# Optimization experiments

Measured on AMD Instinct MI355X. Metric: run time of the kernel, lower is better.

The kernel has to match this reference:

```python
import jax, jax.numpy as jnp
import numpy as np

N_EMBD = 128
N_HEADS = 8
HEAD_SIZE = N_EMBD // N_HEADS  # 16
EPS = 1e-5


def _layernorm(x, g, b):
    m = jnp.mean(x, axis=-1, keepdims=True)
    v = jnp.mean(jnp.square(x - m), axis=-1, keepdims=True)
    return (x - m) * jax.lax.rsqrt(v + EPS) * g + b


def setup_inputs() -> dict:
    key = jax.random.key(0)
    ks = jax.random.split(key, 12)
    B, T, D, H, HS = 16, 1024, N_EMBD, N_HEADS, HEAD_SIZE
    s = 1.0 / np.sqrt(D)
    inp = {
        "x": jax.random.normal(ks[0], (B, T, D), jnp.float32),
        # per-head QKV projections (stacked over heads; matches ModuleList of Linear(D, HS))
        "Wq": jax.random.uniform(ks[1], (H, D, HS), jnp.float32, -s, s),
        "bq": jnp.zeros((H, HS), jnp.float32),
        "Wk": jax.random.uniform(ks[2], (H, D, HS), jnp.float32, -s, s),
        "bk": jnp.zeros((H, HS), jnp.float32),
        "Wv": jax.random.uniform(ks[3], (H, D, HS), jnp.float32, -s, s),
        "bv": jnp.zeros((H, HS), jnp.float32),
        "Wp": jax.random.uniform(ks[4], (H * HS, D), jnp.float32, -s, s),
        "bp": jnp.zeros((D,), jnp.float32),
        "W1": jax.random.uniform(ks[5], (D, 4 * D), jnp.float32, -s, s),
        "b1": jnp.zeros((4 * D,), jnp.float32),
        "W2": jax.random.uniform(ks[6], (4 * D, D), jnp.float32, -1.0 / np.sqrt(4 * D), 1.0 / np.sqrt(4 * D)),
        "b2": jnp.zeros((D,), jnp.float32),
        "g1": jnp.ones((D,), jnp.float32),
        "be1": jnp.zeros((D,), jnp.float32),
        "g2": jnp.ones((D,), jnp.float32),
        "be2": jnp.zeros((D,), jnp.float32),
    }
    return inp


def reference(x, Wq, bq, Wk, bk, Wv, bv, Wp, bp, W1, b1, W2, b2, g1, be1, g2, be2):
    B, T, D = x.shape
    # batched per-head projections: [B,T,D] x [H,D,HS] -> [B,H,T,HS]
    q = jnp.einsum("btd,hds->bhts", x, Wq) + bq[None, :, None, :]
    k = jnp.einsum("btd,hds->bhts", x, Wk) + bk[None, :, None, :]
    v = jnp.einsum("btd,hds->bhts", x, Wv) + bv[None, :, None, :]
    scores = jnp.einsum("bhts,bhus->bhtu", q, k) / np.sqrt(HEAD_SIZE).astype(np.float32)
    tril = jnp.tril(jnp.ones((T, T), x.dtype))
    # faithful to source: multiplicative + additive mask (not -inf where)
    scores = scores * tril - 1e12 * (1.0 - tril)
    attn = jax.nn.softmax(scores, axis=-1)
    out = jnp.einsum("bhtu,bhus->bhts", attn, v)  # [B,H,T,HS]
    # concat heads in head order -> [B,T,H*HS]
    out = out.transpose(0, 2, 1, 3).reshape(B, T, -1)
    attn_out = out @ Wp + bp
    x = _layernorm(attn_out + x, g1, be1)
    h = jax.nn.gelu(x @ W1 + b1, approximate=False) @ W2 + b2
    x = _layernorm(h + x, g2, be2)
    return x
```

## Files before the change

kernel.cpp:

```cpp
#include <hip/hip_runtime.h>
#include <hip/hip_bf16.h>
#include <math.h>

constexpr int NB  = 16;
constexpr int NT  = 1024;
constexpr int ND  = 128;
constexpr int NH  = 8;
constexpr int NHS = 16;
constexpr int NDH = 512;
constexpr long NBT = (long)NB * NT;

typedef __attribute__((ext_vector_type(8))) short short8;
typedef __attribute__((ext_vector_type(4))) float f32x4;
typedef __attribute__((ext_vector_type(4))) unsigned short us4;

__device__ __forceinline__ unsigned short f2bf(float f) {
    __hip_bfloat16 h = __float2bfloat16(f);
    return *(unsigned short*)&h;
}
__device__ __forceinline__ float b2f(unsigned short u) {
    union { unsigned int i; float f; } t;
    t.i = ((unsigned int)u) << 16;
    return t.f;
}

__device__ __forceinline__ short8 cvt8(const float* p) {
    const float4 f0 = *(const float4*)p;
    const float4 f1 = *(const float4*)(p + 4);
    union { short8 s; __hip_bfloat162 h[4]; } u;
    u.h[0] = __float22bfloat162_rn(make_float2(f0.x, f0.y));
    u.h[1] = __float22bfloat162_rn(make_float2(f0.z, f0.w));
    u.h[2] = __float22bfloat162_rn(make_float2(f1.x, f1.y));
    u.h[3] = __float22bfloat162_rn(make_float2(f1.z, f1.w));
    return u.s;
}

__device__ __forceinline__ float fast_gelu(float y) {
    const float t = y * y;
    const float u = __builtin_fmaf(y * 0.044715f, t, y);
    const float e = __builtin_amdgcn_exp2f(u * -2.302118131f);
    return y * __builtin_amdgcn_rcpf(1.0f + e);
}

__global__ __launch_bounds__(256) void k_prep(
    const float* __restrict__ Wq, const float* __restrict__ Wk,
    const float* __restrict__ Wv, __hip_bfloat16* __restrict__ Wqkvt)
{
    const int blk = blockIdx.x, tid = threadIdx.x;
    const int i0 = blk * 1024 + tid * 4;
    const int n = i0 >> 7, d0 = i0 & 127;
    const int sec = n >> 7, m = n & 127;
    const float* W = (sec == 0) ? Wq : (sec == 1) ? Wk : Wv;
    const float* src = W + (m >> 4) * 2048 + (m & 15);
    us4 v;
    #pragma unroll
    for (int j = 0; j < 4; ++j) v[j] = f2bf(src[(d0 + j) * 16]);
    *(us4*)((unsigned short*)Wqkvt + i0) = v;
}

__global__ __launch_bounds__(256) void k_qkv(
    const float* __restrict__ x, const __hip_bfloat16* __restrict__ Wqkvt,
    const float* __restrict__ bq, const float* __restrict__ bk,
    const float* __restrict__ bv,
    const float* __restrict__ Wp, const float* __restrict__ W1,
    const float* __restrict__ W2,
    __hip_bfloat16* __restrict__ Wpt, __hip_bfloat16* __restrict__ W1t,
    __hip_bfloat16* __restrict__ W2t,
    __hip_bfloat16* __restrict__ qo, __hip_bfloat16* __restrict__ ko,
    __hip_bfloat16* __restrict__ vo)
{
    __shared__ __align__(16) unsigned short st[32 * 392];
    const int tid = threadIdx.x;

    if (blockIdx.x >= 512) {
        const int blk = blockIdx.x - 512 + 48;
        us4 v;
        if (blk < 64) {
            const int i0 = (blk - 48) * 1024 + tid * 4;
            const int n = i0 >> 7, d0 = i0 & 127;
            #pragma unroll
            for (int j = 0; j < 4; ++j) v[j] = f2bf(Wp[(d0 + j) * 128 + n]);
            *(us4*)((unsigned short*)Wpt + i0) = v;
        } else if (blk < 128) {
            const int i0 = (blk - 64) * 1024 + tid * 4;
            const int n = i0 >> 7, d0 = i0 & 127;
            #pragma unroll
            for (int j = 0; j < 4; ++j) v[j] = f2bf(W1[(d0 + j) * 512 + n]);
            *(us4*)((unsigned short*)W1t + i0) = v;
        } else {
            const int i0 = (blk - 128) * 1024 + tid * 4;
            const int n = i0 >> 9, k0 = i0 & 511;
            #pragma unroll
            for (int j = 0; j < 4; ++j) v[j] = f2bf(W2[(k0 + j) * 128 + n]);
            *(us4*)((unsigned short*)W2t + i0) = v;
        }
        return;
    }

    const int w    = tid >> 6;
    const int lane = tid & 63;
    const int sL   = lane & 15;
    const int quad = lane >> 4;
    const int tok0 = blockIdx.x * 32;

    const unsigned short* W = (const unsigned short*)Wqkvt;

    short8 bx[2][4];
    #pragma unroll
    for (int tt = 0; tt < 2; ++tt)
        #pragma unroll
        for (int ks = 0; ks < 4; ++ks)
            bx[tt][ks] = cvt8(x + (size_t)(tok0 + tt * 16 + sL) * 128 + ks * 32 + quad * 8);

    f32x4 acc[6][2];
    #pragma unroll
    for (int ci = 0; ci < 6; ++ci)
        #pragma unroll
        for (int tt = 0; tt < 2; ++tt)
            acc[ci][tt] = (f32x4){0.f, 0.f, 0.f, 0.f};

    #pragma unroll
    for (int ks = 0; ks < 4; ++ks) {
        short8 aW[6];
        #pragma unroll
        for (int ci = 0; ci < 6; ++ci) {
            const int ct = w * 6 + ci;
            aW[ci] = *(const short8*)(W + (size_t)(ct * 16 + sL) * 128 + ks * 32 + quad * 8);
        }
        #pragma unroll
        for (int ci = 0; ci < 6; ++ci)
            #pragma unroll
            for (int tt = 0; tt < 2; ++tt)
                acc[ci][tt] = __builtin_amdgcn_mfma_f32_16x16x32_bf16(aW[ci], bx[tt][ks], acc[ci][tt], 0, 0, 0);
    }

    const float qscale = 0.3606737602f;
    #pragma unroll
    for (int ci = 0; ci < 6; ++ci) {
        const int ct = w * 6 + ci;
        const int kind = ct >> 3;
        const int ncc = (ct & 7) * 16 + quad * 4;
        const float4 bb = *(const float4*)(((kind == 0) ? bq : (kind == 1) ? bk : bv) + ncc);
        #pragma unroll
        for (int tt = 0; tt < 2; ++tt) {
            us4 v;
            #pragma unroll
            for (int r = 0; r < 4; ++r) {
                float val = acc[ci][tt][r] + ((const float*)&bb)[r];
                if (kind == 0) val *= qscale;
                v[r] = f2bf(val);
            }
            *(us4*)(st + (tt * 16 + sL) * 392 + ct * 16 + quad * 4) = v;
        }
    }
    __syncthreads();

    const int b = tok0 >> 10, tt0 = tok0 & 1023;
    {
        const int h = tid >> 5, tok = tid & 31;
        const unsigned short* sq = st + tok * 392 + h * 16;
        const unsigned short* sk = st + tok * 392 + 128 + h * 16;
        unsigned short* dq = (unsigned short*)qo + ((size_t)(b * 8 + h) * 1024 + tt0 + tok) * 16;
        unsigned short* dk = (unsigned short*)ko + ((size_t)(b * 8 + h) * 1024 + tt0 + tok) * 16;
        *(short8*)dq       = *(const short8*)sq;
        *(short8*)(dq + 8) = *(const short8*)(sq + 8);
        *(short8*)dk       = *(const short8*)sk;
        *(short8*)(dk + 8) = *(const short8*)(sk + 8);
    }
    if (tid < 128) {
        const int h = tid >> 4, s = tid & 15;
        unsigned short tmp[32];
        #pragma unroll
        for (int tok = 0; tok < 32; ++tok)
            tmp[tok] = st[tok * 392 + 256 + h * 16 + s];
        unsigned short* dv = (unsigned short*)vo + ((size_t)(b * 8 + h) * 16 + s) * 1024 + tt0;
        #pragma unroll
        for (int j = 0; j < 4; ++j)
            *(short8*)(dv + j * 8) = *(const short8*)(tmp + j * 8);
    }
}

__global__ __launch_bounds__(256) void k_attn(
    const __hip_bfloat16* __restrict__ qb, const __hip_bfloat16* __restrict__ kb,
    const __hip_bfloat16* __restrict__ vtb, __hip_bfloat16* __restrict__ att)
{
    const int bh   = blockIdx.x & 127;
    const int sub  = blockIdx.x >> 7;
    const int wave = threadIdx.x >> 6;
    const int lane = threadIdx.x & 63;
    const int sL   = lane & 15;
    const int q    = lane >> 4;
    const int b = bh >> 3, h = bh & 7;
    const int tile = sub * 4 + wave;

    const char* qbase = (const char*)qb  + (size_t)bh * NT * NHS * 2;
    const char* kbase = (const char*)kb  + (size_t)bh * NT * NHS * 2;
    const char* vbase = (const char*)vtb + (size_t)bh * NHS * NT * 2;

    const short8 zz = {0,0,0,0,0,0,0,0};

    const int t0 = tile * 16;
    const int tmy = t0 + sL;

    short8 bQ = zz;
    if (q < 2) bQ = *(const short8*)(qbase + (size_t)tmy * 32 + q * 16);

    f32x4 o = {0.f, 0.f, 0.f, 0.f};
    float lp = 0.f;

    const int nch = (t0 + 47) >> 5;
    for (int c = 0; c < nch; ++c) {
        const int u0 = c * 32;
        short8 aK0 = zz, aK1 = zz;
        if (q < 2) {
            aK0 = *(const short8*)(kbase + (size_t)(u0 + sL) * 32 + q * 16);
            aK1 = *(const short8*)(kbase + (size_t)(u0 + 16 + sL) * 32 + q * 16);
        }
        const f32x4 zc = {0.f, 0.f, 0.f, 0.f};
        f32x4 sT0 = __builtin_amdgcn_mfma_f32_16x16x32_bf16(aK0, bQ, zc, 0, 0, 0);
        f32x4 sT1 = __builtin_amdgcn_mfma_f32_16x16x32_bf16(aK1, bQ, zc, 0, 0, 0);

        int pk[4];
        if (u0 + 31 <= t0) {
            #pragma unroll
            for (int r = 0; r < 4; ++r) {
                const float p0 = __builtin_amdgcn_exp2f(sT0[r]);
                const float p1 = __builtin_amdgcn_exp2f(sT1[r]);
                lp += p0 + p1;
                __hip_bfloat162 hh = __float22bfloat162_rn(make_float2(p0, p1));
                pk[r] = *(int*)&hh;
            }
        } else {
            #pragma unroll
            for (int r = 0; r < 4; ++r) {
                const int ua = u0 + 4 * q + r;
                const float e0 = __builtin_amdgcn_exp2f(sT0[r]);
                const float e1 = __builtin_amdgcn_exp2f(sT1[r]);
                const float p0 = (ua      <= tmy) ? e0 : 0.f;
                const float p1 = (ua + 16 <= tmy) ? e1 : 0.f;
                lp += p0 + p1;
                __hip_bfloat162 hh = __float22bfloat162_rn(make_float2(p0, p1));
                pk[r] = *(int*)&hh;
            }
        }

        short8 bP;
        #pragma unroll
        for (int j = 0; j < 8; ++j) {
            const int srcq = ((q & 1) << 1) + (j >> 2);
            const int src  = (srcq << 4) + sL;
            const int g = __shfl(pk[j & 3], src);
            bP[j] = (short)((q < 2) ? (g & 0xffff) : ((unsigned)g >> 16));
        }

        const short8 aV = *(const short8*)(vbase + ((size_t)sL * NT + u0 + q * 8) * 2);
        o = __builtin_amdgcn_mfma_f32_16x16x32_bf16(aV, bP, o, 0, 0, 0);
    }

    float l = lp;
    l += __shfl_xor(l, 16);
    l += __shfl_xor(l, 32);
    const float inv = 1.0f / l;
    us4 res;
    res[0] = f2bf(o[0] * inv); res[1] = f2bf(o[1] * inv);
    res[2] = f2bf(o[2] * inv); res[3] = f2bf(o[3] * inv);
    *(us4*)((unsigned short*)att + ((size_t)b * NT + tmy) * ND + h * NHS + q * 4) = res;
}

__global__ __launch_bounds__(256) void k_tail(
    const __hip_bfloat16* __restrict__ attb, const __hip_bfloat16* __restrict__ Wpt,
    const __hip_bfloat16* __restrict__ W1t, const __hip_bfloat16* __restrict__ W2t,
    const float* __restrict__ x, const float* __restrict__ bp,
    const float* __restrict__ g1, const float* __restrict__ be1,
    const float* __restrict__ b1, const float* __restrict__ b2,
    const float* __restrict__ g2, const float* __restrict__ be2,
    float* __restrict__ out)
{
    __shared__ __align__(16) unsigned short buf[32 * 528];
    __shared__ __align__(16) unsigned short l1b[32 * 136];
    float* ysA           = (float*)buf;
    unsigned short* midb = buf;
    float* ys2           = (float*)buf;
    const int w    = threadIdx.x >> 6;
    const int lane = threadIdx.x & 63;
    const int sL   = lane & 15;
    const int quad = lane >> 4;
    const int tok0 = blockIdx.x * 32;

    {
        const unsigned short* A = (const unsigned short*)attb;
        const unsigned short* W = (const unsigned short*)Wpt;
        short8 bfr[2][4];
        #pragma unroll
        for (int tt = 0; tt < 2; ++tt)
            #pragma unroll
            for (int ks = 0; ks < 4; ++ks)
                bfr[tt][ks] = *(const short8*)(A + (size_t)(tok0 + tt * 16 + sL) * 128 + ks * 32 + quad * 8);

        f32x4 acc[2][2];
        #pragma unroll
        for (int ci = 0; ci < 2; ++ci)
            #pragma unroll
            for (int tt = 0; tt < 2; ++tt)
                acc[ci][tt] = (f32x4){0.f, 0.f, 0.f, 0.f};

        #pragma unroll
        for (int ks = 0; ks < 4; ++ks) {
            short8 aW[2];
            #pragma unroll
            for (int ci = 0; ci < 2; ++ci)
                aW[ci] = *(const short8*)(W + (size_t)((w * 2 + ci) * 16 + sL) * 128 + ks * 32 + quad * 8);
            #pragma unroll
            for (int ci = 0; ci < 2; ++ci)
                #pragma unroll
                for (int tt = 0; tt < 2; ++tt)
                    acc[ci][tt] = __builtin_amdgcn_mfma_f32_16x16x32_bf16(aW[ci], bfr[tt][ks], acc[ci][tt], 0, 0, 0);
        }
        #pragma unroll
        for (int ci = 0; ci < 2; ++ci) {
            const int n0 = (w * 2 + ci) * 16 + quad * 4;
            const float4 bb = *(const float4*)(bp + n0);
            #pragma unroll
            for (int tt = 0; tt < 2; ++tt) {
                float4 v;
                v.x = acc[ci][tt][0] + bb.x; v.y = acc[ci][tt][1] + bb.y;
                v.z = acc[ci][tt][2] + bb.z; v.w = acc[ci][tt][3] + bb.w;
                *(float4*)(ysA + (size_t)(tt * 16 + sL) * 132 + n0) = v;
            }
        }
    }
    __syncthreads();

    const int tok = threadIdx.x >> 3;
    const int l8  = threadIdx.x & 7;
    const int c0  = l8 * 16;
    {
        float vals[16];
        float s = 0.f, s2 = 0.f;
        #pragma unroll
        for (int ch = 0; ch < 4; ++ch) {
            const float4 ly = *(const float4*)(ysA + (size_t)tok * 132 + c0 + ch * 4);
            const float4 gx = *(const float4*)(x + (size_t)(tok0 + tok) * 128 + c0 + ch * 4);
            vals[ch*4+0] = ly.x + gx.x; vals[ch*4+1] = ly.y + gx.y;
            vals[ch*4+2] = ly.z + gx.z; vals[ch*4+3] = ly.w + gx.w;
            #pragma unroll
            for (int j = 0; j < 4; ++j) { s += vals[ch*4+j]; s2 += vals[ch*4+j] * vals[ch*4+j]; }
        }
        #pragma unroll
        for (int off = 1; off <= 4; off <<= 1) {
            s  += __shfl_xor(s, off, 8);
            s2 += __shfl_xor(s2, off, 8);
        }
        const float mean = s * (1.0f / 128.0f);
        const float var  = s2 * (1.0f / 128.0f) - mean * mean;
        const float rstd = rsqrtf(var + 1e-5f);
        #pragma unroll
        for (int ch = 0; ch < 4; ++ch) {
            const float4 gg = *(const float4*)(g1 + c0 + ch * 4);
            const float4 bb = *(const float4*)(be1 + c0 + ch * 4);
            const float ln0  = (vals[ch*4+0] - mean) * rstd * gg.x + bb.x;
            const float ln1v = (vals[ch*4+1] - mean) * rstd * gg.y + bb.y;
            const float ln2v = (vals[ch*4+2] - mean) * rstd * gg.z + bb.z;
            const float ln3  = (vals[ch*4+3] - mean) * rstd * gg.w + bb.w;
            us4 lb;
            lb[0] = f2bf(ln0); lb[1] = f2bf(ln1v); lb[2] = f2bf(ln2v); lb[3] = f2bf(ln3);
            *(us4*)(l1b + tok * 136 + c0 + ch * 4) = lb;
        }
    }
    __syncthreads();

    {
        const unsigned short* W = (const unsigned short*)W1t;
        short8 bl[2][4];
        #pragma unroll
        for (int tt = 0; tt < 2; ++tt)
            #pragma unroll
            for (int ks = 0; ks < 4; ++ks)
                bl[tt][ks] = *(const short8*)(l1b + (tt * 16 + sL) * 136 + ks * 32 + quad * 8);

        f32x4 acc[8][2];
        #pragma unroll
        for (int ci = 0; ci < 8; ++ci)
            #pragma unroll
            for (int tt = 0; tt < 2; ++tt)
                acc[ci][tt] = (f32x4){0.f, 0.f, 0.f, 0.f};

        #pragma unroll
        for (int ks = 0; ks < 4; ++ks) {
            short8 aW[8];
            #pragma unroll
            for (int ci = 0; ci < 8; ++ci)
                aW[ci] = *(const short8*)(W + (size_t)((w * 8 + ci) * 16 + sL) * 128 + ks * 32 + quad * 8);
            #pragma unroll
            for (int ci = 0; ci < 8; ++ci)
                #pragma unroll
                for (int tt = 0; tt < 2; ++tt)
                    acc[ci][tt] = __builtin_amdgcn_mfma_f32_16x16x32_bf16(aW[ci], bl[tt][ks], acc[ci][tt], 0, 0, 0);
        }
        #pragma unroll
        for (int ci = 0; ci < 8; ++ci) {
            const int n0 = (w * 8 + ci) * 16 + quad * 4;
            const float4 bb = *(const float4*)(b1 + n0);
            #pragma unroll
            for (int tt = 0; tt < 2; ++tt) {
                us4 v;
                v[0] = f2bf(fast_gelu(acc[ci][tt][0] + bb.x));
                v[1] = f2bf(fast_gelu(acc[ci][tt][1] + bb.y));
                v[2] = f2bf(fast_gelu(acc[ci][tt][2] + bb.z));
                v[3] = f2bf(fast_gelu(acc[ci][tt][3] + bb.w));
                *(us4*)(midb + (tt * 16 + sL) * 528 + n0) = v;
            }
        }
    }
    __syncthreads();

    f32x4 acc2[2][2];
    #pragma unroll
    for (int ci = 0; ci < 2; ++ci)
        #pragma unroll
        for (int tt = 0; tt < 2; ++tt)
            acc2[ci][tt] = (f32x4){0.f, 0.f, 0.f, 0.f};
    {
        const unsigned short* W = (const unsigned short*)W2t;
        #pragma unroll
        for (int ks = 0; ks < 16; ++ks) {
            const short8 bm0 = *(const short8*)(midb + (size_t)sL * 528 + ks * 32 + quad * 8);
            const short8 bm1 = *(const short8*)(midb + (size_t)(16 + sL) * 528 + ks * 32 + quad * 8);
            const short8 aW0 = *(const short8*)(W + (size_t)((w * 2) * 16 + sL) * 512 + ks * 32 + quad * 8);
            const short8 aW1 = *(const short8*)(W + (size_t)((w * 2 + 1) * 16 + sL) * 512 + ks * 32 + quad * 8);
            acc2[0][0] = __builtin_amdgcn_mfma_f32_16x16x32_bf16(aW0, bm0, acc2[0][0], 0, 0, 0);
            acc2[0][1] = __builtin_amdgcn_mfma_f32_16x16x32_bf16(aW0, bm1, acc2[0][1], 0, 0, 0);
            acc2[1][0] = __builtin_amdgcn_mfma_f32_16x16x32_bf16(aW1, bm0, acc2[1][0], 0, 0, 0);
            acc2[1][1] = __builtin_amdgcn_mfma_f32_16x16x32_bf16(aW1, bm1, acc2[1][1], 0, 0, 0);
        }
    }
    __syncthreads();
    #pragma unroll
    for (int ci = 0; ci < 2; ++ci) {
        const int n0 = (w * 2 + ci) * 16 + quad * 4;
        const float4 bb = *(const float4*)(b2 + n0);
        #pragma unroll
        for (int tt = 0; tt < 2; ++tt) {
            float4 v;
            v.x = acc2[ci][tt][0] + bb.x; v.y = acc2[ci][tt][1] + bb.y;
            v.z = acc2[ci][tt][2] + bb.z; v.w = acc2[ci][tt][3] + bb.w;
            *(float4*)(ys2 + (size_t)(tt * 16 + sL) * 132 + n0) = v;
        }
    }
    __syncthreads();

    {
        float vals[16];
        float s = 0.f, s2 = 0.f;
        #pragma unroll
        for (int ch = 0; ch < 4; ++ch) {
            const float4 ly = *(const float4*)(ys2 + (size_t)tok * 132 + c0 + ch * 4);
            const us4 lb = *(const us4*)(l1b + tok * 136 + c0 + ch * 4);
            vals[ch*4+0] = ly.x + b2f(lb[0]); vals[ch*4+1] = ly.y + b2f(lb[1]);
            vals[ch*4+2] = ly.z + b2f(lb[2]); vals[ch*4+3] = ly.w + b2f(lb[3]);
            #pragma unroll
            for (int j = 0; j < 4; ++j) { s += vals[ch*4+j]; s2 += vals[ch*4+j] * vals[ch*4+j]; }
        }
        #pragma unroll
        for (int off = 1; off <= 4; off <<= 1) {
            s  += __shfl_xor(s, off, 8);
            s2 += __shfl_xor(s2, off, 8);
        }
        const float mean = s * (1.0f / 128.0f);
        const float var  = s2 * (1.0f / 128.0f) - mean * mean;
        const float rstd = rsqrtf(var + 1e-5f);
        #pragma unroll
        for (int ch = 0; ch < 4; ++ch) {
            const float4 gg = *(const float4*)(g2 + c0 + ch * 4);
            const float4 bb = *(const float4*)(be2 + c0 + ch * 4);
            float4 ln;
            ln.x = (vals[ch*4+0] - mean) * rstd * gg.x + bb.x;
            ln.y = (vals[ch*4+1] - mean) * rstd * gg.y + bb.y;
            ln.z = (vals[ch*4+2] - mean) * rstd * gg.z + bb.z;
            ln.w = (vals[ch*4+3] - mean) * rstd * gg.w + bb.w;
            *(float4*)(out + (size_t)(tok0 + tok) * 128 + c0 + ch * 4) = ln;
        }
    }
}

extern "C" void kernel_launch(void* const* d_in, const int* in_sizes, int n_in,
                              void* d_out, int out_size, void* d_ws, size_t ws_size,
                              hipStream_t stream)
{
    (void)in_sizes; (void)n_in; (void)out_size; (void)ws_size;
    const float* x   = (const float*)d_in[0];
    const float* Wq  = (const float*)d_in[1];
    const float* bq  = (const float*)d_in[2];
    const float* Wk  = (const float*)d_in[3];
    const float* bk  = (const float*)d_in[4];
    const float* Wv  = (const float*)d_in[5];
    const float* bv  = (const float*)d_in[6];
    const float* Wp  = (const float*)d_in[7];
    const float* bp  = (const float*)d_in[8];
    const float* W1  = (const float*)d_in[9];
    const float* b1  = (const float*)d_in[10];
    const float* W2  = (const float*)d_in[11];
    const float* b2  = (const float*)d_in[12];
    const float* g1  = (const float*)d_in[13];
    const float* be1 = (const float*)d_in[14];
    const float* g2  = (const float*)d_in[15];
    const float* be2 = (const float*)d_in[16];
    float* out = (float*)d_out;

    char* wsb = (char*)d_ws;
    __hip_bfloat16* qb   = (__hip_bfloat16*)wsb;
    __hip_bfloat16* kb   = (__hip_bfloat16*)(wsb + (4u  << 20));
    __hip_bfloat16* vtb  = (__hip_bfloat16*)(wsb + (8u  << 20));
    __hip_bfloat16* attb = (__hip_bfloat16*)(wsb + (12u << 20));
    __hip_bfloat16* Wqkvt= (__hip_bfloat16*)(wsb + (16u << 20));
    __hip_bfloat16* Wpt  = (__hip_bfloat16*)(wsb + (16u << 20) + (96u  << 10));
    __hip_bfloat16* W1t  = (__hip_bfloat16*)(wsb + (16u << 20) + (128u << 10));
    __hip_bfloat16* W2t  = (__hip_bfloat16*)(wsb + (16u << 20) + (256u << 10));

    k_prep<<<48,   256, 0, stream>>>(Wq, Wk, Wv, Wqkvt);
    k_qkv <<<656,  256, 0, stream>>>(x, Wqkvt, bq, bk, bv, Wp, W1, W2,
                                     Wpt, W1t, W2t, qb, kb, vtb);
    k_attn<<<2048, 256, 0, stream>>>(qb, kb, vtb, attb);
    k_tail<<<512,  256, 0, stream>>>(attb, Wpt, W1t, W2t, x, bp, g1, be1,
                                     b1, b2, g2, be2, out);
}
```

Before: 164.2 us.

## Switch causal attention to 32x32x16 MFMA with 32-query tiles per wave

The attention kernel now computes scores for 32 queries by 32 keys per wave using the 32x32x16 bf16 MFMA, instead of two 16x16x32 MFMAs that left half the lanes zero-padded. The P·V product becomes two 32x32 MFMAs over the same accumulator. The grid is halved and tiles are interleaved across waves (tile = wave*8 + sub) to spread causal work evenly across blocks. The aim is to stop wasting MFMA lanes on the 16-wide head dimension and to cut per-chunk shuffle and mask overhead. In exchange it uses more accumulator registers, has fewer waves in flight, and relies on correct indexing of the 32x32 output layout for the causal mask and the stores.

Result: no change. 165.3 us (+0.7%).

```diff
diff --git a/kernel.cpp b/kernel.cpp
--- a/kernel.cpp
+++ b/kernel.cpp
@@ -12,6 +12,7 @@
 
 typedef __attribute__((ext_vector_type(8))) short short8;
 typedef __attribute__((ext_vector_type(4))) float f32x4;
+typedef __attribute__((ext_vector_type(16))) float f32x16;
 typedef __attribute__((ext_vector_type(4))) unsigned short us4;
 
 __device__ __forceinline__ unsigned short f2bf(float f) {
@@ -188,83 +189,86 @@
     const int sub  = blockIdx.x >> 7;
     const int wave = threadIdx.x >> 6;
     const int lane = threadIdx.x & 63;
-    const int sL   = lane & 15;
-    const int q    = lane >> 4;
-    const int b = bh >> 3, h = bh & 7;
-    const int tile = sub * 4 + wave;
+    const int ln31 = lane & 31;
+    const int h    = lane >> 5;
+    const int b = bh >> 3, hd = bh & 7;
+    const int tile = wave * 8 + sub;
 
     const char* qbase = (const char*)qb  + (size_t)bh * NT * NHS * 2;
     const char* kbase = (const char*)kb  + (size_t)bh * NT * NHS * 2;
     const char* vbase = (const char*)vtb + (size_t)bh * NHS * NT * 2;
 
-    const short8 zz = {0,0,0,0,0,0,0,0};
-
-    const int t0 = tile * 16;
-    const int tmy = t0 + sL;
-
-    short8 bQ = zz;
-    if (q < 2) bQ = *(const short8*)(qbase + (size_t)tmy * 32 + q * 16);
-
-    f32x4 o = {0.f, 0.f, 0.f, 0.f};
+    const int t0 = tile * 32;
+    const int tmy = t0 + ln31;
+    const int sv  = lane & 15;
+
+    const short8 bQ = *(const short8*)(qbase + (size_t)tmy * 32 + h * 16);
+
+    f32x16 o;
+    #pragma unroll
+    for (int r = 0; r < 16; ++r) o[r] = 0.f;
     float lp = 0.f;
 
-    const int nch = (t0 + 47) >> 5;
-    for (int c = 0; c < nch; ++c) {
+    for (int c = 0; c <= tile; ++c) {
         const int u0 = c * 32;
-        short8 aK0 = zz, aK1 = zz;
-        if (q < 2) {
-            aK0 = *(const short8*)(kbase + (size_t)(u0 + sL) * 32 + q * 16);
-            aK1 = *(const short8*)(kbase + (size_t)(u0 + 16 + sL) * 32 + q * 16);
-        }
-        const f32x4 zc = {0.f, 0.f, 0.f, 0.f};
-        f32x4 sT0 = __builtin_amdgcn_mfma_f32_16x16x32_bf16(aK0, bQ, zc, 0, 0, 0);
-        f32x4 sT1 = __builtin_amdgcn_mfma_f32_16x16x32_bf16(aK1, bQ, zc, 0, 0, 0);
-
-        int pk[4];
-        if (u0 + 31 <= t0) {
-            #pragma unroll
-            for (int r = 0; r < 4; ++r) {
-                const float p0 = __builtin_amdgcn_exp2f(sT0[r]);
-                const float p1 = __builtin_amdgcn_exp2f(sT1[r]);
+        const short8 aK = *(const short8*)(kbase + (size_t)(u0 + ln31) * 32 + h * 16);
+        f32x16 zc;
+        #pragma unroll
+        for (int r = 0; r < 16; ++r) zc[r] = 0.f;
+        f32x16 sT = __builtin_amdgcn_mfma_f32_32x32x16_bf16(aK, bQ, zc, 0, 0, 0);
+
+        int pk[8];
+        if (c < tile) {
+            #pragma unroll
+            for (int r = 0; r < 8; ++r) {
+                const float p0 = __builtin_amdgcn_exp2f(sT[r]);
+                const float p1 = __builtin_amdgcn_exp2f(sT[r + 8]);
                 lp += p0 + p1;
                 __hip_bfloat162 hh = __float22bfloat162_rn(make_float2(p0, p1));
                 pk[r] = *(int*)&hh;
             }
         } else {
             #pragma unroll
-            for (int r = 0; r < 4; ++r) {
-                const int ua = u0 + 4 * q + r;
-                const float e0 = __builtin_amdgcn_exp2f(sT0[r]);
-                const float e1 = __builtin_amdgcn_exp2f(sT1[r]);
-                const float p0 = (ua      <= tmy) ? e0 : 0.f;
-                const float p1 = (ua + 16 <= tmy) ? e1 : 0.f;
+            for (int r = 0; r < 8; ++r) {
+                const int row0 = (r & 3) + 8 * (r >> 2) + 4 * h;
+                const float e0 = __builtin_amdgcn_exp2f(sT[r]);
+                const float e1 = __builtin_amdgcn_exp2f(sT[r + 8]);
+                const float p0 = (row0      <= ln31) ? e0 : 0.f;
+                const float p1 = (row0 + 16 <= ln31) ? e1 : 0.f;
                 lp += p0 + p1;
                 __hip_bfloat162 hh = __float22bfloat162_rn(make_float2(p0, p1));
                 pk[r] = *(int*)&hh;
             }
         }
 
-        short8 bP;
+        short8 bP1, bP2;
         #pragma unroll
         for (int j = 0; j < 8; ++j) {
-            const int srcq = ((q & 1) << 1) + (j >> 2);
-            const int src  = (srcq << 4) + sL;
-            const int g = __shfl(pk[j & 3], src);
-            bP[j] = (short)((q < 2) ? (g & 0xffff) : ((unsigned)g >> 16));
-        }
-
-        const short8 aV = *(const short8*)(vbase + ((size_t)sL * NT + u0 + q * 8) * 2);
-        o = __builtin_amdgcn_mfma_f32_16x16x32_bf16(aV, bP, o, 0, 0, 0);
-    }
-
-    float l = lp;
-    l += __shfl_xor(l, 16);
-    l += __shfl_xor(l, 32);
+            const int src = ln31 + ((j >= 4) ? 32 : 0);
+            const int gA = __shfl(pk[j & 3], src);
+            const int gB = __shfl(pk[(j & 3) + 4], src);
+            const int g  = h ? gB : gA;
+            bP1[j] = (short)(g & 0xffff);
+            bP2[j] = (short)((unsigned)g >> 16);
+        }
+
+        const short8 aV1 = *(const short8*)(vbase + ((size_t)sv * NT + u0 + h * 8) * 2);
+        const short8 aV2 = *(const short8*)(vbase + ((size_t)sv * NT + u0 + 16 + h * 8) * 2);
+        o = __builtin_amdgcn_mfma_f32_32x32x16_bf16(aV1, bP1, o, 0, 0, 0);
+        o = __builtin_amdgcn_mfma_f32_32x32x16_bf16(aV2, bP2, o, 0, 0, 0);
+    }
+
+    float l = lp + __shfl_xor(lp, 32);
     const float inv = 1.0f / l;
-    us4 res;
-    res[0] = f2bf(o[0] * inv); res[1] = f2bf(o[1] * inv);
-    res[2] = f2bf(o[2] * inv); res[3] = f2bf(o[3] * inv);
-    *(us4*)((unsigned short*)att + ((size_t)b * NT + tmy) * ND + h * NHS + q * 4) = res;
+
+    unsigned short* dst = (unsigned short*)att + ((size_t)b * NT + tmy) * ND + hd * NHS;
+    us4 r0, r1;
+    r0[0] = f2bf(o[0] * inv); r0[1] = f2bf(o[1] * inv);
+    r0[2] = f2bf(o[2] * inv); r0[3] = f2bf(o[3] * inv);
+    r1[0] = f2bf(o[4] * inv); r1[1] = f2bf(o[5] * inv);
+    r1[2] = f2bf(o[6] * inv); r1[3] = f2bf(o[7] * inv);
+    *(us4*)(dst + 4 * h)     = r0;
+    *(us4*)(dst + 8 + 4 * h) = r1;
 }
 
 __global__ __launch_bounds__(256) void k_tail(
@@ -520,7 +524,7 @@
     k_prep<<<48,   256, 0, stream>>>(Wq, Wk, Wv, Wqkvt);
     k_qkv <<<656,  256, 0, stream>>>(x, Wqkvt, bq, bk, bv, Wp, W1, W2,
                                      Wpt, W1t, W2t, qb, kb, vtb);
-    k_attn<<<2048, 256, 0, stream>>>(qb, kb, vtb, attb);
+    k_attn<<<1024, 256, 0, stream>>>(qb, kb, vtb, attb);
     k_tail<<<512,  256, 0, stream>>>(attb, Wpt, W1t, W2t, x, bp, g1, be1,
                                      b1, b2, g2, be2, out);
 }
```
